# Kernel optimization log

Measured on AMD Instinct MI355X. Metric: run time of the kernel, lower is better.

The kernel has to match this reference:

```python
import jax, jax.numpy as jnp
import numpy as np

ALPHA = 0.01
TOP_K = 2
N_EXPERTS = 8

def setup_inputs() -> dict:
    key = jax.random.key(0)
    k1, k2 = jax.random.split(key)
    hidden_states = jax.random.normal(k1, (4, 4096, 2048), dtype=jnp.float32)
    # kaiming_uniform_(a=sqrt(5)) on [E, H] -> bound = sqrt(6/((1+5)*H)) = 1/sqrt(H)
    bound = 1.0 / np.sqrt(2048.0)
    weight = jax.random.uniform(k2, (N_EXPERTS, 2048), dtype=jnp.float32,
                                minval=-bound, maxval=bound)
    return {"hidden_states": hidden_states, "weight": weight}

def reference(hidden_states, weight):
    bsz, seq_len, h = hidden_states.shape
    x = hidden_states.reshape(-1, h)                      # [T, H], T = bsz*seq_len
    logits = jnp.einsum('th,eh->te', x, weight)           # [T, E]
    scores = jax.nn.softmax(logits, axis=-1)              # [T, E]
    topk_weight, topk_idx = jax.lax.top_k(scores, TOP_K)  # [T, K], [T, K]
    # aux load-balancing loss (training, seq_aux=False)
    flat_idx = topk_idx.reshape(-1)                       # [T*K]
    counts = jnp.zeros((N_EXPERTS,), dtype=jnp.float32).at[flat_idx].add(1.0)
    ce = counts / flat_idx.shape[0]                       # mean of one-hots
    Pi = scores.mean(axis=0)                              # [E]
    fi = ce * N_EXPERTS
    aux_loss = jnp.sum(Pi * fi) * ALPHA
    return topk_idx, topk_weight, aux_loss
```

## Files before the change

### kernel.cpp

```cpp
#include <hip/hip_runtime.h>

#define T_TOK 16384
#define H 2048
#define NE 8
#define TPG 4
#define ALPHA 0.01f
#define TOPK 2
#define NBLK 1024


__global__ __launch_bounds__(256) void gate_main(
    const float* __restrict__ x, const float* __restrict__ w,
    float* __restrict__ out, float* __restrict__ ws)
{
    __shared__ float s_pi[NE];
    __shared__ float s_cnt[NE];
    const int tid = threadIdx.x;
    if (tid < NE) { s_pi[tid] = 0.f; s_cnt[tid] = 0.f; }
    __syncthreads();

    const int lane = tid & 63;
    const int wave = tid >> 6;
    const int gw   = blockIdx.x * 4 + wave;
    const int t0   = gw * TPG;

    float acc[NE][TPG];
#pragma unroll
    for (int e = 0; e < NE; e++)
#pragma unroll
        for (int t = 0; t < TPG; t++) acc[e][t] = 0.f;

    const float4* __restrict__ xv = (const float4*)x;
    const float4* __restrict__ wv = (const float4*)w;

#pragma unroll
    for (int j = 0; j < 8; j++) {
        const int c4 = j * 64 + lane;
        float4 xr[TPG];
#pragma unroll
        for (int t = 0; t < TPG; t++)
            xr[t] = xv[(size_t)(t0 + t) * (H / 4) + c4];
#pragma unroll
        for (int e = 0; e < NE; e++) {
            const float4 wr = wv[e * (H / 4) + c4];
#pragma unroll
            for (int t = 0; t < TPG; t++) {
                acc[e][t] = fmaf(xr[t].x, wr.x, acc[e][t]);
                acc[e][t] = fmaf(xr[t].y, wr.y, acc[e][t]);
                acc[e][t] = fmaf(xr[t].z, wr.z, acc[e][t]);
                acc[e][t] = fmaf(xr[t].w, wr.w, acc[e][t]);
            }
        }
    }

#pragma unroll
    for (int e = 0; e < NE; e++)
#pragma unroll
        for (int t = 0; t < TPG; t++) {
            float v = acc[e][t];
#pragma unroll
            for (int off = 32; off >= 1; off >>= 1)
                v += __shfl_xor(v, off, 64);
            acc[e][t] = v;
        }

    float pi_loc[NE], cnt_loc[NE];
#pragma unroll
    for (int e = 0; e < NE; e++) { pi_loc[e] = 0.f; cnt_loc[e] = 0.f; }

#pragma unroll
    for (int t = 0; t < TPG; t++) {
        float l[NE];
#pragma unroll
        for (int e = 0; e < NE; e++) l[e] = acc[e][t];
        float m = l[0];
#pragma unroll
        for (int e = 1; e < NE; e++) m = fmaxf(m, l[e]);
        float s[NE];
        float sum = 0.f;
#pragma unroll
        for (int e = 0; e < NE; e++) { s[e] = expf(l[e] - m); sum += s[e]; }
#pragma unroll
        for (int e = 0; e < NE; e++) s[e] = s[e] / sum;

        float b1 = -1.f, b2 = -1.f;
        int   i1 = 0,    i2 = 0;
#pragma unroll
        for (int e = 0; e < NE; e++) {
            if (s[e] > b1) { b2 = b1; i2 = i1; b1 = s[e]; i1 = e; }
            else if (s[e] > b2) { b2 = s[e]; i2 = e; }
        }

        if (lane == t) {
            const int tok = t0 + t;
            out[tok * 2 + 0]             = (float)i1;
            out[tok * 2 + 1]             = (float)i2;
            out[2 * T_TOK + tok * 2 + 0] = b1;
            out[2 * T_TOK + tok * 2 + 1] = b2;
        }
        const float sel = (lane == t) ? 1.f : 0.f;
#pragma unroll
        for (int e = 0; e < NE; e++) {
            pi_loc[e]  += sel * s[e];
            cnt_loc[e] += sel * (((i1 == e) ? 1.f : 0.f) + ((i2 == e) ? 1.f : 0.f));
        }
    }

    if (lane < TPG) {
#pragma unroll
        for (int e = 0; e < NE; e++) {
            atomicAdd(&s_pi[e],  pi_loc[e]);
            atomicAdd(&s_cnt[e], cnt_loc[e]);
        }
    }
    __syncthreads();
    if (tid < NE) {
        ws[blockIdx.x * 16 + tid]     = s_pi[tid];
        ws[blockIdx.x * 16 + 8 + tid] = s_cnt[tid];
    }
}

__global__ __launch_bounds__(256) void gate_aux(
    const float* __restrict__ ws, float* __restrict__ out)
{
    __shared__ float s_pi[NE];
    __shared__ float s_cnt[NE];
    const int tid = threadIdx.x;
    if (tid < NE) { s_pi[tid] = 0.f; s_cnt[tid] = 0.f; }
    __syncthreads();

    float pi[NE], cnt[NE];
#pragma unroll
    for (int e = 0; e < NE; e++) { pi[e] = 0.f; cnt[e] = 0.f; }

    for (int b = tid; b < NBLK; b += 256) {
        const float4* p = (const float4*)(ws + b * 16);
        float4 a0 = p[0], a1 = p[1], a2 = p[2], a3 = p[3];
        pi[0] += a0.x; pi[1] += a0.y; pi[2] += a0.z; pi[3] += a0.w;
        pi[4] += a1.x; pi[5] += a1.y; pi[6] += a1.z; pi[7] += a1.w;
        cnt[0] += a2.x; cnt[1] += a2.y; cnt[2] += a2.z; cnt[3] += a2.w;
        cnt[4] += a3.x; cnt[5] += a3.y; cnt[6] += a3.z; cnt[7] += a3.w;
    }

#pragma unroll
    for (int e = 0; e < NE; e++) {
#pragma unroll
        for (int off = 32; off >= 1; off >>= 1) {
            pi[e]  += __shfl_xor(pi[e],  off, 64);
            cnt[e] += __shfl_xor(cnt[e], off, 64);
        }
    }
    if ((tid & 63) == 0) {
#pragma unroll
        for (int e = 0; e < NE; e++) {
            atomicAdd(&s_pi[e],  pi[e]);
            atomicAdd(&s_cnt[e], cnt[e]);
        }
    }
    __syncthreads();

    if (tid == 0) {
        float aux = 0.f;
#pragma unroll
        for (int e = 0; e < NE; e++) {
            const float Pi = s_pi[e] / (float)T_TOK;
            const float ce = s_cnt[e] / (float)(T_TOK * TOPK);
            aux += Pi * ce * (float)NE;
        }
        out[4 * T_TOK] = aux * ALPHA;
    }
}

extern "C" void kernel_launch(void* const* d_in, const int* in_sizes, int n_in,
                              void* d_out, int out_size, void* d_ws, size_t ws_size,
                              hipStream_t stream) {
    const float* x = (const float*)d_in[0];
    const float* w = (const float*)d_in[1];
    float* out = (float*)d_out;
    float* ws  = (float*)d_ws;

    gate_main<<<NBLK, 256, 0, stream>>>(x, w, out, ws);
    gate_aux<<<1, 256, 0, stream>>>(ws, out);
}
```

Before: 217.4 us.

## Stage gate weights in LDS and double-buffer activation loads with larger blocks

Each block now loads the full 8x2048 gate weight matrix into shared memory once, then reads weights from LDS instead of global/L2. Activation loads are software-pipelined: the next column chunk of x is fetched while the current one is being multiplied. Blocks grow to 512 threads covering 8 waves with half the grid, and the softmax switches to the fast __expf intrinsic. The 64 KB LDS footprint per block limits occupancy, and __expf trades a little accuracy for speed.

```diff
diff --git a/kernel.cpp b/kernel.cpp
--- a/kernel.cpp
+++ b/kernel.cpp
@@ -2,53 +2,78 @@
 
 #define T_TOK 16384
 #define H 2048
+#define HV (H / 4)
 #define NE 8
 #define TPG 4
+#define WPB 8
 #define ALPHA 0.01f
 #define TOPK 2
-#define NBLK 1024
-
-
-__global__ __launch_bounds__(256) void gate_main(
+#define NBLK 512
+
+
+__global__ __launch_bounds__(512, 4) void gate_main(
     const float* __restrict__ x, const float* __restrict__ w,
     float* __restrict__ out, float* __restrict__ ws)
 {
+    __shared__ float wl[NE * H];
     __shared__ float s_pi[NE];
     __shared__ float s_cnt[NE];
-    const int tid = threadIdx.x;
-    if (tid < NE) { s_pi[tid] = 0.f; s_cnt[tid] = 0.f; }
-    __syncthreads();
-
+
+    const int tid  = threadIdx.x;
     const int lane = tid & 63;
     const int wave = tid >> 6;
-    const int gw   = blockIdx.x * 4 + wave;
-    const int t0   = gw * TPG;
-
-    float acc[NE][TPG];
-#pragma unroll
-    for (int e = 0; e < NE; e++)
-#pragma unroll
-        for (int t = 0; t < TPG; t++) acc[e][t] = 0.f;
+    const int t0   = (blockIdx.x * WPB + wave) * TPG;
 
     const float4* __restrict__ xv = (const float4*)x;
     const float4* __restrict__ wv = (const float4*)w;
 
-#pragma unroll
-    for (int j = 0; j < 8; j++) {
-        const int c4 = j * 64 + lane;
-        float4 xr[TPG];
-#pragma unroll
-        for (int t = 0; t < TPG; t++)
-            xr[t] = xv[(size_t)(t0 + t) * (H / 4) + c4];
-#pragma unroll
-        for (int e = 0; e < NE; e++) {
-            const float4 wr = wv[e * (H / 4) + c4];
+    const float4* xp = xv + (size_t)t0 * HV + lane;
+    float4 xa[TPG], xb[TPG];
+#pragma unroll
+    for (int t = 0; t < TPG; t++) xa[t] = xp[t * HV];
+
+    float4* wl4 = (float4*)wl;
+#pragma unroll
+    for (int k = 0; k < 8; k++) wl4[tid + k * 512] = wv[tid + k * 512];
+    if (tid < NE) { s_pi[tid] = 0.f; s_cnt[tid] = 0.f; }
+    __syncthreads();
+
+    float acc[NE][TPG];
+#pragma unroll
+    for (int e = 0; e < NE; e++)
+#pragma unroll
+        for (int t = 0; t < TPG; t++) acc[e][t] = 0.f;
+
+    const float4* wlv = (const float4*)wl;
+
+#pragma unroll
+    for (int j = 0; j < 8; j += 2) {
+#pragma unroll
+        for (int t = 0; t < TPG; t++) xb[t] = xp[t * HV + (j + 1) * 64];
+#pragma unroll
+        for (int e = 0; e < NE; e++) {
+            const float4 wr = wlv[e * HV + j * 64 + lane];
 #pragma unroll
             for (int t = 0; t < TPG; t++) {
-                acc[e][t] = fmaf(xr[t].x, wr.x, acc[e][t]);
-                acc[e][t] = fmaf(xr[t].y, wr.y, acc[e][t]);
-                acc[e][t] = fmaf(xr[t].z, wr.z, acc[e][t]);
-                acc[e][t] = fmaf(xr[t].w, wr.w, acc[e][t]);
+                acc[e][t] = fmaf(xa[t].x, wr.x, acc[e][t]);
+                acc[e][t] = fmaf(xa[t].y, wr.y, acc[e][t]);
+                acc[e][t] = fmaf(xa[t].z, wr.z, acc[e][t]);
+                acc[e][t] = fmaf(xa[t].w, wr.w, acc[e][t]);
+            }
+        }
+        if (j + 2 < 8) {
+#pragma unroll
+            for (int t = 0; t < TPG; t++) xa[t] = xp[t * HV + (j + 2) * 64];
+        }
+#pragma unroll
+        for (int e = 0; e < NE; e++) {
+            const float4 wr = wlv[e * HV + (j + 1) * 64 + lane];
+#pragma unroll
+            for (int t = 0; t < TPG; t++) {
+                acc[e][t] = fmaf(xb[t].x, wr.x, acc[e][t]);
+                acc[e][t] = fmaf(xb[t].y, wr.y, acc[e][t]);
+                acc[e][t] = fmaf(xb[t].z, wr.z, acc[e][t]);
+                acc[e][t] = fmaf(xb[t].w, wr.w, acc[e][t]);
             }
         }
     }
@@ -79,7 +104,7 @@
         float s[NE];
         float sum = 0.f;
 #pragma unroll
-        for (int e = 0; e < NE; e++) { s[e] = expf(l[e] - m); sum += s[e]; }
+        for (int e = 0; e < NE; e++) { s[e] = __expf(l[e] - m); sum += s[e]; }
 #pragma unroll
         for (int e = 0; e < NE; e++) s[e] = s[e] / sum;
 
@@ -179,6 +204,6 @@
     float* out = (float*)d_out;
     float* ws  = (float*)d_ws;
 
-    gate_main<<<NBLK, 256, 0, stream>>>(x, w, out, ws);
+    gate_main<<<NBLK, 512, 0, stream>>>(x, w, out, ws);
     gate_aux<<<1, 256, 0, stream>>>(ws, out);
 }
```

Measured after the change: 203.4 us. 1.07x faster.

## Prefetch all token rows into registers and stage gate weights in LDS

Applied to the files above, without the earlier changes.

Each wave now issues all 32 float4 loads for its four tokens up front, so more memory requests are in flight at once, instead of loading per column chunk. The whole 8x2048 weight matrix (64 KB) is copied into shared memory per block, and launch bounds request two blocks per CU. Softmax switches to fast __expf and a hardware reciprocal. The costs are much higher register pressure (128 VGPRs just for x), a 64 KB LDS footprint per block that limits occupancy, and slightly less accurate softmax.

```diff
diff --git a/kernel.cpp b/kernel.cpp
--- a/kernel.cpp
+++ b/kernel.cpp
@@ -2,6 +2,7 @@
 
 #define T_TOK 16384
 #define H 2048
+#define HV (H / 4)
 #define NE 8
 #define TPG 4
 #define ALPHA 0.01f
@@ -9,20 +10,34 @@
 #define NBLK 1024
 
 
-__global__ __launch_bounds__(256) void gate_main(
+__global__ __launch_bounds__(256, 2) void gate_main(
     const float* __restrict__ x, const float* __restrict__ w,
     float* __restrict__ out, float* __restrict__ ws)
 {
+    __shared__ float4 wl[NE * HV];
     __shared__ float s_pi[NE];
     __shared__ float s_cnt[NE];
-    const int tid = threadIdx.x;
+
+    const int tid  = threadIdx.x;
+    const int lane = tid & 63;
+    const int wave = tid >> 6;
+    const int t0   = (blockIdx.x * 4 + wave) * TPG;
+
+    const float4* __restrict__ xv = (const float4*)x;
+    const float4* __restrict__ wv = (const float4*)w;
+
+    const float4* xp = xv + (size_t)t0 * HV + lane;
+    float4 xr[8][TPG];
+#pragma unroll
+    for (int j = 0; j < 8; j++)
+#pragma unroll
+        for (int t = 0; t < TPG; t++)
+            xr[j][t] = xp[t * HV + j * 64];
+
+#pragma unroll
+    for (int k = 0; k < 16; k++) wl[tid + k * 256] = wv[tid + k * 256];
     if (tid < NE) { s_pi[tid] = 0.f; s_cnt[tid] = 0.f; }
     __syncthreads();
-
-    const int lane = tid & 63;
-    const int wave = tid >> 6;
-    const int gw   = blockIdx.x * 4 + wave;
-    const int t0   = gw * TPG;
 
     float acc[NE][TPG];
 #pragma unroll
@@ -30,25 +45,17 @@
 #pragma unroll
         for (int t = 0; t < TPG; t++) acc[e][t] = 0.f;
 
-    const float4* __restrict__ xv = (const float4*)x;
-    const float4* __restrict__ wv = (const float4*)w;
-
 #pragma unroll
     for (int j = 0; j < 8; j++) {
-        const int c4 = j * 64 + lane;
-        float4 xr[TPG];
-#pragma unroll
-        for (int t = 0; t < TPG; t++)
-            xr[t] = xv[(size_t)(t0 + t) * (H / 4) + c4];
 #pragma unroll
         for (int e = 0; e < NE; e++) {
-            const float4 wr = wv[e * (H / 4) + c4];
+            const float4 wr = wl[e * HV + j * 64 + lane];
 #pragma unroll
             for (int t = 0; t < TPG; t++) {
-                acc[e][t] = fmaf(xr[t].x, wr.x, acc[e][t]);
-                acc[e][t] = fmaf(xr[t].y, wr.y, acc[e][t]);
-                acc[e][t] = fmaf(xr[t].z, wr.z, acc[e][t]);
-                acc[e][t] = fmaf(xr[t].w, wr.w, acc[e][t]);
+                acc[e][t] = fmaf(xr[j][t].x, wr.x, acc[e][t]);
+                acc[e][t] = fmaf(xr[j][t].y, wr.y, acc[e][t]);
+                acc[e][t] = fmaf(xr[j][t].z, wr.z, acc[e][t]);
+                acc[e][t] = fmaf(xr[j][t].w, wr.w, acc[e][t]);
             }
         }
     }
@@ -79,9 +86,10 @@
         float s[NE];
         float sum = 0.f;
 #pragma unroll
-        for (int e = 0; e < NE; e++) { s[e] = expf(l[e] - m); sum += s[e]; }
+        for (int e = 0; e < NE; e++) { s[e] = __expf(l[e] - m); sum += s[e]; }
+        const float rs = __builtin_amdgcn_rcpf(sum);
 #pragma unroll
-        for (int e = 0; e < NE; e++) s[e] = s[e] / sum;
+        for (int e = 0; e < NE; e++) s[e] = s[e] * rs;
 
         float b1 = -1.f, b2 = -1.f;
         int   i1 = 0,    i2 = 0;
```

Result: faster. 205.0 us (-5.7%).
